# Performance work log

Hardware: AMD Instinct MI355X
Metric: run time of the kernel (lower is better)

## Reference

```python
import jax, jax.numpy as jnp
import numpy as np


def conv2d(x, w, b=None, pad=0):
    out = jax.lax.conv_general_dilated(x, w, (1, 1), [(pad, pad), (pad, pad)],
                                       dimension_numbers=('NCHW', 'OIHW', 'NCHW'))
    if b is not None:
        out = out + b[None, :, None, None]
    return out


def resb(x, w1, w2):
    y = conv2d(x, w1, pad=1)
    y = jnp.where(y > 0, y, 0.1 * y)  # LeakyReLU(0.1)
    y = conv2d(y, w2, pad=1)
    return y + x


def fepam(Q, S, R, px, py):
    # Q: (b,C,h,w); S: (b,C,H,W); R: (b,vC,H,W); px,py: (b,h,w,k) int coords into (H,W)
    b, C, h, w = Q.shape
    Ws = S.shape[3]
    vC = R.shape[1]
    k = px.shape[-1]
    idx = (px.reshape(b, -1) * Ws + py.reshape(b, -1))  # (b, h*w*k) flat spatial index
    Key = jnp.take_along_axis(S.reshape(b, C, -1), idx[:, None, :], axis=2).reshape(b, C, h * w, k)
    Val = jnp.take_along_axis(R.reshape(b, vC, -1), idx[:, None, :], axis=2).reshape(b, vC, h * w, k)
    Qv = Q.transpose(0, 2, 3, 1).reshape(b, h * w, C)
    score = jnp.einsum('bqc,bcqk->bqk', Qv, Key)          # (b, h*w, k)
    attn = jax.nn.softmax(score, axis=-1)
    buf = jnp.einsum('bqk,bvqk->bqv', attn, Val)          # (b, h*w, vC)
    return buf.reshape(b, h, w, vC).transpose(0, 3, 1, 2)


def setup_inputs() -> dict:
    key = jax.random.key(0)
    ks = jax.random.split(key, 24)
    b, C, h, w = 2, 32, 128, 128
    H, W = 512, 512
    ct, cout, kk = 16, 32, 64
    s = 0.05
    inp = {
        'lr0': jax.random.normal(ks[0], (b, C, h, w), jnp.float32),
        'lr1': jax.random.normal(ks[1], (b, C, h, w), jnp.float32),
        'lr2': jax.random.normal(ks[2], (b, C, h, w), jnp.float32),
        'hr_in': jax.random.normal(ks[3], (b, C, H, W), jnp.float32),
        'wl1': jax.random.normal(ks[4], (C, C, 3, 3), jnp.float32) * s,
        'wl2': jax.random.normal(ks[5], (C, C, 3, 3), jnp.float32) * s,
        'wh1': jax.random.normal(ks[6], (C, C, 3, 3), jnp.float32) * s,
        'wh2': jax.random.normal(ks[7], (C, C, 3, 3), jnp.float32) * s,
        'wq': jax.random.normal(ks[8], (ct, C, 1, 1), jnp.float32) * s,
        'bq': jax.random.normal(ks[9], (ct,), jnp.float32) * s,
        'wk': jax.random.normal(ks[10], (ct, C, 1, 1), jnp.float32) * s,
        'bk': jax.random.normal(ks[11], (ct,), jnp.float32) * s,
        'whk': jax.random.normal(ks[12], (ct, C, 1, 1), jnp.float32) * s,
        'bhk': jax.random.normal(ks[13], (ct,), jnp.float32) * s,
        'wf': jax.random.normal(ks[14], (cout, C * 3 + C, 1, 1), jnp.float32) * s,
        'bf': jax.random.normal(ks[15], (cout,), jnp.float32) * s,
        'px0': jax.random.randint(ks[16], (b, h, w, kk), 0, h, jnp.int64),
        'py0': jax.random.randint(ks[17], (b, h, w, kk), 0, w, jnp.int64),
        'px1': jax.random.randint(ks[18], (b, h, w, kk), 0, h, jnp.int64),
        'py1': jax.random.randint(ks[19], (b, h, w, kk), 0, w, jnp.int64),
        'px2': jax.random.randint(ks[20], (b, h, w, kk), 0, H, jnp.int64),
        'py2': jax.random.randint(ks[21], (b, h, w, kk), 0, W, jnp.int64),
        'is_training': 1,
    }
    return inp


def reference(lr0, lr1, lr2, hr_in, wl1, wl2, wh1, wh2, wq, bq, wk, bk, whk, bhk, wf, bf,
              px0, py0, px1, py1, px2, py2, is_training):
    lb0 = resb(lr0, wl1, wl2)
    lb1 = resb(lr1, wl1, wl2)
    lb2 = resb(lr2, wl1, wl2)
    hb = resb(hr_in, wh1, wh2)
    Q = conv2d(lb0, wq, bq)
    S1 = conv2d(lb1, wk, bk)
    S2 = conv2d(lb2, wk, bk)
    S3 = conv2d(hb, whk, bhk)
    b1 = fepam(Q, S1, lr1, px0, py0)
    b2 = fepam(Q, S2, lr2, px1, py1)
    b3 = fepam(Q, S3, hr_in, px2, py2)
    out = conv2d(jnp.concatenate([b1, b2, b3, lb0], axis=1), wf, bf)
    return out
```

## Files before the change

### kernel.cpp

```cpp
#include <hip/hip_runtime.h>
#include <hip/hip_bf16.h>

typedef short bfv8 __attribute__((ext_vector_type(8)));
typedef float f4v __attribute__((ext_vector_type(4)));
typedef float f2v __attribute__((ext_vector_type(2)));

static __device__ __forceinline__ unsigned short f2bf(float f) {
  unsigned u = __float_as_uint(f);
  unsigned r = (u + 0x7FFFu + ((u >> 16) & 1u)) >> 16;
  return (unsigned short)r;
}
static __device__ __forceinline__ unsigned pack2bf(float lo, float hi) {
  return (unsigned)f2bf(lo) | ((unsigned)f2bf(hi) << 16);
}
static __device__ __forceinline__ unsigned pack4fp8(float a, float b, float c, float d) {
  int w = __builtin_amdgcn_cvt_pk_fp8_f32(a, b, 0, 0);
  w = __builtin_amdgcn_cvt_pk_fp8_f32(c, d, w, 1);
  return (unsigned)w;
}


struct B3  { const unsigned short* p[3]; };
struct F3  { const float* p[3]; };
struct OB3 { unsigned short* p[3]; };
struct OF3 { float* p[3]; };
struct OC3 { unsigned char* p[3]; };

__global__ __launch_bounds__(256) void wconv_bf16_kernel(
    const float* __restrict__ wl1, const float* __restrict__ wl2,
    const float* __restrict__ wh1, const float* __restrict__ wh2,
    const float* __restrict__ whk, const float* __restrict__ wq,
    const float* __restrict__ wk,
    unsigned short* __restrict__ ol1, unsigned short* __restrict__ ol2,
    unsigned short* __restrict__ oh1, unsigned short* __restrict__ oh2,
    unsigned short* __restrict__ ok, unsigned short* __restrict__ oq,
    unsigned short* __restrict__ okk,
    const int* __restrict__ pxprobe, int* __restrict__ flag)
{
  int i = blockIdx.x * 256 + threadIdx.x;
  int y = blockIdx.y;
  if (y < 4) {
    const float* w = y == 0 ? wl1 : y == 1 ? wl2 : y == 2 ? wh1 : wh2;
    unsigned short* o = y == 0 ? ol1 : y == 1 ? ol2 : y == 2 ? oh1 : oh2;
    if (i < 9216) {
      int t = i / 1024, rem = i % 1024, co = rem >> 5, ci = rem & 31;
      o[i] = f2bf(w[(co * 32 + ci) * 9 + t]);
    }
  } else if (y == 4) {
    if (i < 512) ok[i] = f2bf(whk[i]);
    else if (i < 1024) oq[i - 512] = f2bf(wq[i - 512]);
    else if (i < 1536) okk[i - 1024] = f2bf(wk[i - 1024]);
  } else if (blockIdx.x == 0) {
    __shared__ int s;
    if (threadIdx.x == 0) s = 0;
    __syncthreads();
    if (pxprobe[2 * threadIdx.x + 1] != 0) atomicOr(&s, 1);
    __syncthreads();
    if (threadIdx.x == 0) *flag = (s == 0) ? 1 : 0;
  }
}

__global__ __launch_bounds__(256) void hrc_kernel(
    const float* __restrict__ x, unsigned short* __restrict__ o,
    unsigned char* __restrict__ kv)
{
  int p = blockIdx.x * 256 + threadIdx.x;
  int bb = p >> 18, pp = p & 262143;
  const float* xb = x + ((size_t)bb * 32) * 262144 + pp;
  float f[32];
  unsigned short v[32];
#pragma unroll
  for (int c = 0; c < 32; ++c) { f[c] = xb[(size_t)c * 262144]; v[c] = f2bf(f[c]); }
  uint4* op = (uint4*)(o + (size_t)p * 32);
#pragma unroll
  for (int q = 0; q < 4; ++q) op[q] = ((uint4*)v)[q];
  unsigned w8[8];
#pragma unroll
  for (int d = 0; d < 8; ++d)
    w8[d] = pack4fp8(f[4 * d], f[4 * d + 1], f[4 * d + 2], f[4 * d + 3]);
  uint4* o8p = (uint4*)(kv + (size_t)p * 64 + 16);
  o8p[0] = ((uint4*)w8)[0];
  o8p[1] = ((uint4*)w8)[1];
}

__global__ __launch_bounds__(256) void lrprep_kernel(F3 xs, OB3 ob, OC3 kvs)
{
  int tn = blockIdx.y;
  int p = blockIdx.x * 256 + threadIdx.x;
  int bb = p >> 14, pp = p & 16383;
  const float* xb = xs.p[tn] + ((size_t)bb * 32) * 16384 + pp;
  float f[32];
  unsigned short v[32];
#pragma unroll
  for (int c = 0; c < 32; ++c) { f[c] = xb[(size_t)c * 16384]; v[c] = f2bf(f[c]); }
  uint4* bp = (uint4*)(ob.p[tn] + (size_t)p * 32);
#pragma unroll
  for (int q = 0; q < 4; ++q) bp[q] = ((uint4*)v)[q];
  unsigned char* kv = kvs.p[tn];
  if (kv) {
    unsigned w8[8];
#pragma unroll
    for (int d = 0; d < 8; ++d)
      w8[d] = pack4fp8(f[4 * d], f[4 * d + 1], f[4 * d + 2], f[4 * d + 3]);
    uint4* o8p = (uint4*)(kv + (size_t)p * 64 + 16);
    o8p[0] = ((uint4*)w8)[0];
    o8p[1] = ((uint4*)w8)[1];
  }
}

template <int N, int MODE>
__global__ __launch_bounds__(256, 2) void conv_mfma_kernel(
    B3 xs, const unsigned short* __restrict__ WB, B3 resb,
    B3 pwb, F3 pbias, OB3 outb, OF3 outf)
{
  __shared__ uint4 smem_[2640];
  unsigned char* smem = (unsigned char*)smem_;
  const int NN = N * N;
  const int bx0 = blockIdx.x * 64, by0 = blockIdx.y * 8;
  const int tn = (N == 512) ? 0 : (blockIdx.z >> 1);
  const int bb = (N == 512) ? blockIdx.z : (blockIdx.z & 1);
  const int tid = threadIdx.x;
  const int w = tid >> 6, lane = tid & 63;
  const int l15 = lane & 15, ch = lane >> 4;

  bfv8 wa[9][2];
#pragma unroll
  for (int t = 0; t < 9; ++t)
#pragma unroll
    for (int j = 0; j < 2; ++j)
      wa[t][j] = *(const bfv8*)(WB + t * 1024 + (16 * j + l15) * 32 + ch * 8);

  const unsigned short* Xb = xs.p[tn] + (size_t)bb * NN * 32;
  for (int g = tid; g < 2640; g += 256) {
    int row = g / 264, rem = g - row * 264;
    int px = rem >> 2, c4 = rem & 3;
    int gy = by0 + row - 1, gx = bx0 + px - 1;
    uint4 v = {0u, 0u, 0u, 0u};
    if (gy >= 0 && gy < N && gx >= 0 && gx < N)
      v = *(const uint4*)(Xb + (size_t)(gy * N + gx) * 32 + c4 * 8);
    int byt = (row * 4224 + px * 64 + c4 * 16) ^ ((px & 7) << 4);
    *(uint4*)(smem + byt) = v;
  }
  __syncthreads();

  f4v acc[2][8];
#pragma unroll
  for (int j = 0; j < 2; ++j)
#pragma unroll
    for (int f = 0; f < 8; ++f) acc[j][f] = (f4v){0.f, 0.f, 0.f, 0.f};

#pragma unroll
  for (int dy = 0; dy < 3; ++dy)
#pragma unroll
    for (int dx = 0; dx < 3; ++dx)
#pragma unroll
      for (int f = 0; f < 8; ++f) {
        const int hrow = 2 * w + (f >> 2) + dy;
        const int xh = 16 * (f & 3) + l15 + dx;
        const int byt = (hrow * 4224 + xh * 64 + ch * 16) ^ ((xh & 7) << 4);
        bfv8 b = *(bfv8*)(smem + byt);
        acc[0][f] = __builtin_amdgcn_mfma_f32_16x16x32_bf16(wa[dy * 3 + dx][0], b, acc[0][f], 0, 0, 0);
        acc[1][f] = __builtin_amdgcn_mfma_f32_16x16x32_bf16(wa[dy * 3 + dx][1], b, acc[1][f], 0, 0, 0);
      }

  if (MODE == 0) {
    unsigned short* ob = outb.p[tn] + (size_t)bb * NN * 32;
#pragma unroll
    for (int j = 0; j < 2; ++j)
#pragma unroll
      for (int f = 0; f < 8; ++f) {
        const int gy = by0 + 2 * w + (f >> 2);
        const int gx = bx0 + 16 * (f & 3) + l15;
        const int co0 = 16 * j + ch * 4;
        unsigned short o[4];
#pragma unroll
        for (int i = 0; i < 4; ++i) {
          float a = acc[j][f][i];
          a = a > 0.f ? a : 0.1f * a;
          o[i] = f2bf(a);
        }
        *(uint2*)(ob + (size_t)(gy * N + gx) * 32 + co0) = *(uint2*)o;
      }
  } else {
    const unsigned short* rb = resb.p[tn] + (size_t)bb * NN * 32;
#pragma unroll
    for (int j = 0; j < 2; ++j)
#pragma unroll
      for (int f = 0; f < 8; ++f) {
        const int gy = by0 + 2 * w + (f >> 2);
        const int gx = bx0 + 16 * (f & 3) + l15;
        const int co0 = 16 * j + ch * 4;
        uint2 r = *(const uint2*)(rb + (size_t)(gy * N + gx) * 32 + co0);
        acc[j][f][0] += __uint_as_float(r.x << 16);
        acc[j][f][1] += __uint_as_float(r.x & 0xFFFF0000u);
        acc[j][f][2] += __uint_as_float(r.y << 16);
        acc[j][f][3] += __uint_as_float(r.y & 0xFFFF0000u);
      }
    if (MODE == 3 && tn == 0) {
      float* lb = outf.p[0] + (size_t)bb * NN * 32;
#pragma unroll
      for (int j = 0; j < 2; ++j)
#pragma unroll
        for (int f = 0; f < 8; ++f) {
          const int gy = by0 + 2 * w + (f >> 2);
          const int gx = bx0 + 16 * (f & 3) + l15;
          const int co0 = 16 * j + ch * 4;
          float o[4] = {acc[j][f][0], acc[j][f][1], acc[j][f][2], acc[j][f][3]};
          *(float4*)(lb + (size_t)(gy * N + gx) * 32 + co0) = *(float4*)o;
        }
    }
    __syncthreads();
#pragma unroll
    for (int j = 0; j < 2; ++j)
#pragma unroll
      for (int f = 0; f < 8; ++f) {
        const int rl = 2 * w + (f >> 2);
        const int xl = 16 * (f & 3) + l15;
        const int co0 = 16 * j + ch * 4;
        unsigned short o[4];
#pragma unroll
        for (int i = 0; i < 4; ++i) o[i] = f2bf(acc[j][f][i]);
        int byt = ((rl * 4096 + xl * 64 + ((co0 >> 3) << 4)) ^ ((xl & 7) << 4)) + (co0 & 7) * 2;
        *(uint2*)(smem + byt) = *(uint2*)o;
      }
    __syncthreads();
    bfv8 pka = *(const bfv8*)(pwb.p[tn] + l15 * 32 + ch * 8);
    float4 bv = *(const float4*)(pbias.p[tn] + ch * 4);
#pragma unroll
    for (int f = 0; f < 8; ++f) {
      const int rl = 2 * w + (f >> 2);
      const int xl = 16 * (f & 3) + l15;
      const int byt = (rl * 4096 + xl * 64 + ch * 16) ^ ((xl & 7) << 4);
      bfv8 b = *(bfv8*)(smem + byt);
      f4v a2 = __builtin_amdgcn_mfma_f32_16x16x32_bf16(pka, b, (f4v){0.f, 0.f, 0.f, 0.f}, 0, 0, 0);
      const int gy = by0 + rl, gx = bx0 + xl;
      if (MODE == 3 && tn == 0) {
        float* Pq = outf.p[1] + (size_t)bb * ((size_t)NN * 16);
        float o[4] = {a2[0] + bv.x, a2[1] + bv.y, a2[2] + bv.z, a2[3] + bv.w};
        *(float4*)(Pq + (size_t)(gy * N + gx) * 16 + ch * 4) = *(float4*)o;
      } else {
        unsigned char* KV = (unsigned char*)outb.p[tn];
        unsigned wd = pack4fp8(a2[0] + bv.x, a2[1] + bv.y, a2[2] + bv.z, a2[3] + bv.w);
        *(unsigned*)(KV + ((size_t)bb * NN + (size_t)(gy * N + gx)) * 64 + ch * 4) = wd;
      }
    }
  }
}

__global__ __launch_bounds__(256) void fepam_kernel(
    const float* __restrict__ Qt, const unsigned char* __restrict__ KV,
    const int* __restrict__ px, const int* __restrict__ py,
    const int* __restrict__ idxflag, float* __restrict__ out, int Ws, int HWs)
{
  __shared__ unsigned pv[4][64][17];
  const int wv = threadIdx.x >> 6;
  const int lane = threadIdx.x & 63;
  const int wid = (blockIdx.x * 256 + threadIdx.x) >> 6;
  const int bb = wid >> 14;
  const int f = *idxflag;
  const int j = (wid * 64 + lane) << f;
  const int sidx = px[j] * Ws + py[j];

  const unsigned char* rec = KV + ((size_t)bb * HWs + sidx) * 64;
  uint4 kw  = *(const uint4*)rec;
  uint4 vw0 = *(const uint4*)(rec + 16);
  uint4 vw1 = *(const uint4*)(rec + 32);

  const float* qp = Qt + (size_t)wid * 16;
  float qreg[16];
#pragma unroll
  for (int q = 0; q < 4; ++q) ((float4*)qreg)[q] = ((const float4*)qp)[q];

  unsigned karr[4] = {kw.x, kw.y, kw.z, kw.w};
  float score = 0.f;
#pragma unroll
  for (int d = 0; d < 4; ++d) {
    f2v lo = __builtin_amdgcn_cvt_pk_f32_fp8((int)karr[d], 0);
    f2v hi = __builtin_amdgcn_cvt_pk_f32_fp8((int)karr[d], 1);
    score = fmaf(qreg[4 * d],     lo[0], score);
    score = fmaf(qreg[4 * d + 1], lo[1], score);
    score = fmaf(qreg[4 * d + 2], hi[0], score);
    score = fmaf(qreg[4 * d + 3], hi[1], score);
  }
  float e = __expf(fminf(score, 80.f));
  float s = e;
#pragma unroll
  for (int off = 32; off; off >>= 1) s += __shfl_xor(s, off);

  unsigned varr[8] = {vw0.x, vw0.y, vw0.z, vw0.w, vw1.x, vw1.y, vw1.z, vw1.w};
#pragma unroll
  for (int d = 0; d < 8; ++d) {
    f2v lo = __builtin_amdgcn_cvt_pk_f32_fp8((int)varr[d], 0);
    f2v hi = __builtin_amdgcn_cvt_pk_f32_fp8((int)varr[d], 1);
    unsigned ulo0 = __float_as_uint(e * lo[0]) + 0x8000u;
    unsigned ulo1 = __float_as_uint(e * lo[1]) + 0x8000u;
    unsigned uhi0 = __float_as_uint(e * hi[0]) + 0x8000u;
    unsigned uhi1 = __float_as_uint(e * hi[1]) + 0x8000u;
    pv[wv][lane][2 * d]     = (ulo0 >> 16) | (ulo1 & 0xFFFF0000u);
    pv[wv][lane][2 * d + 1] = (uhi0 >> 16) | (uhi1 & 0xFFFF0000u);
  }
  __syncthreads();

  const int c = lane & 31, h = lane >> 5;
  const int wsel = c >> 1;
  const unsigned sh = (c & 1) ? 0u : 16u;
  float val = 0.f;
#pragma unroll
  for (int i = 0; i < 32; ++i) {
    unsigned u = pv[wv][h * 32 + i][wsel];
    val += __uint_as_float((u << sh) & 0xFFFF0000u);
  }
  val += __shfl_xor(val, 32);
  if (lane < 32) out[(size_t)wid * 32 + c] = val / s;
}

__global__ __launch_bounds__(256) void final_conv_kernel(
    const float* __restrict__ bt1, const float* __restrict__ bt2,
    const float* __restrict__ bt3, const float* __restrict__ lb0,
    const float* __restrict__ wf, const float* __restrict__ bfb,
    float* __restrict__ out)
{
  __shared__ uint4 smem_[1544];
  unsigned char* smem = (unsigned char*)smem_;
  const int tid = threadIdx.x;
  const int px0 = blockIdx.x * 64;

  {
    const int pxl = tid >> 2, c0 = (tid & 3) * 8;
    const float* srcs[4] = {bt1, bt2, bt3, lb0};
#pragma unroll
    for (int q = 0; q < 4; ++q) {
      const float* sp = srcs[q] + (size_t)(px0 + pxl) * 32 + c0;
      float4 a = ((const float4*)sp)[0];
      float4 b = ((const float4*)sp)[1];
      unsigned pk[4] = {pack2bf(a.x, a.y), pack2bf(a.z, a.w),
                        pack2bf(b.x, b.y), pack2bf(b.z, b.w)};
      int byt = (pxl * 256 + q * 64 + c0 * 2) ^ ((pxl & 7) << 4);
      *(uint4*)(smem + byt) = *(uint4*)pk;
    }
    const int co = tid >> 3, cw = (tid & 7) * 16;
    const float* wp = wf + co * 128 + cw;
    float4 w0 = ((const float4*)wp)[0], w1 = ((const float4*)wp)[1];
    float4 w2 = ((const float4*)wp)[2], w3 = ((const float4*)wp)[3];
    unsigned pk0[4] = {pack2bf(w0.x, w0.y), pack2bf(w0.z, w0.w),
                       pack2bf(w1.x, w1.y), pack2bf(w1.z, w1.w)};
    unsigned pk1[4] = {pack2bf(w2.x, w2.y), pack2bf(w2.z, w2.w),
                       pack2bf(w3.x, w3.y), pack2bf(w3.z, w3.w)};
    int b0 = 16384 + ((co * 256 + cw * 2) ^ ((co & 7) << 4));
    int b1 = 16384 + ((co * 256 + cw * 2 + 16) ^ ((co & 7) << 4));
    *(uint4*)(smem + b0) = *(uint4*)pk0;
    *(uint4*)(smem + b1) = *(uint4*)pk1;
    if (tid < 32) *(float*)(smem + 24576 + tid * 4) = bfb[tid];
  }
  __syncthreads();

  const int w = tid >> 6, lane = tid & 63;
  const int l15 = lane & 15, ch = lane >> 4;
  const int pxl = w * 16 + l15;

  f4v acc[2] = {(f4v){0.f, 0.f, 0.f, 0.f}, (f4v){0.f, 0.f, 0.f, 0.f}};
#pragma unroll
  for (int kb = 0; kb < 4; ++kb) {
    bfv8 b = *(bfv8*)(smem + ((pxl * 256 + kb * 64 + ch * 16) ^ ((pxl & 7) << 4)));
#pragma unroll
    for (int j = 0; j < 2; ++j) {
      const int co = 16 * j + l15;
      bfv8 a = *(bfv8*)(smem + 16384 + ((co * 256 + kb * 64 + ch * 16) ^ ((co & 7) << 4)));
      acc[j] = __builtin_amdgcn_mfma_f32_16x16x32_bf16(a, b, acc[j], 0, 0, 0);
    }
  }

  const int p = px0 + pxl;
  const int bb = p >> 14, pp = p & 16383;
#pragma unroll
  for (int j = 0; j < 2; ++j)
#pragma unroll
    for (int i = 0; i < 4; ++i) {
      const int co = 16 * j + ch * 4 + i;
      float bias = *(float*)(smem + 24576 + co * 4);
      out[((size_t)(bb * 32 + co)) * 16384 + pp] = acc[j][i] + bias;
    }
}

extern "C" void kernel_launch(void* const* d_in, const int* in_sizes, int n_in,
                              void* d_out, int out_size, void* d_ws, size_t ws_size,
                              hipStream_t stream)
{
  const float* lr0 = (const float*)d_in[0];
  const float* lr1 = (const float*)d_in[1];
  const float* lr2 = (const float*)d_in[2];
  const float* hr  = (const float*)d_in[3];
  const float* wl1 = (const float*)d_in[4];
  const float* wl2 = (const float*)d_in[5];
  const float* wh1 = (const float*)d_in[6];
  const float* wh2 = (const float*)d_in[7];
  const float* wq  = (const float*)d_in[8];
  const float* bq  = (const float*)d_in[9];
  const float* wk  = (const float*)d_in[10];
  const float* bk  = (const float*)d_in[11];
  const float* whk = (const float*)d_in[12];
  const float* bhk = (const float*)d_in[13];
  const float* wf  = (const float*)d_in[14];
  const float* bf  = (const float*)d_in[15];
  const int* px0 = (const int*)d_in[16];
  const int* py0 = (const int*)d_in[17];
  const int* px1 = (const int*)d_in[18];
  const int* py1 = (const int*)d_in[19];
  const int* px2 = (const int*)d_in[20];
  const int* py2 = (const int*)d_in[21];
  float* out = (float*)d_out;
  float* ws = (float*)d_ws;

  unsigned char*  KV3 = (unsigned char*)ws;
  unsigned short* YC  = (unsigned short*)(ws + 8388608);
  unsigned short* HRC = (unsigned short*)(ws + 16777216);
  unsigned short* LRC = (unsigned short*)(ws + 25165824);
  unsigned short* YLC = (unsigned short*)(ws + 26738688);
  unsigned char*  KV1 = (unsigned char*)(ws + 28311552);
  unsigned char*  KV2 = (unsigned char*)(ws + 28835840);
  float* QT  = ws + 29360128;
  float* LB0 = ws + 30408704;
  float* BT1 = ws + 33030144;
  float* BT2 = ws + 34078720;
  float* BT3 = ws + 35127296;
  unsigned short* WBL1 = (unsigned short*)(ws + 36175872);
  unsigned short* WBL2 = (unsigned short*)(ws + 36180480);
  unsigned short* WBH1 = (unsigned short*)(ws + 36185088);
  unsigned short* WBH2 = (unsigned short*)(ws + 36189696);
  unsigned short* WHKB = (unsigned short*)(ws + 36194304);
  unsigned short* WQB  = (unsigned short*)(ws + 36194560);
  unsigned short* WKB  = (unsigned short*)(ws + 36194816);
  int* IDXFLAG = (int*)(ws + 36195072);

  unsigned short* LRC0 = LRC;
  unsigned short* LRC1 = LRC + 1048576;
  unsigned short* LRC2 = LRC + 2097152;
  unsigned short* YLC0 = YLC;
  unsigned short* YLC1 = YLC + 1048576;
  unsigned short* YLC2 = YLC + 2097152;

  B3 bnone{};
  F3 fnone{};
  OB3 obnone{};
  OF3 ofnone{};

  static hipStream_t s2 = nullptr;
  static hipEvent_t eA = nullptr, eB = nullptr, eS = nullptr;
  if (s2 == nullptr) {
    hipStreamCreateWithFlags(&s2, hipStreamNonBlocking);
    hipEventCreateWithFlags(&eA, hipEventDisableTiming);
    hipEventCreateWithFlags(&eB, hipEventDisableTiming);
    hipEventCreateWithFlags(&eS, hipEventDisableTiming);
  }

  wconv_bf16_kernel<<<dim3(36, 6), 256, 0, stream>>>(
      wl1, wl2, wh1, wh2, whk, wq, wk,
      WBL1, WBL2, WBH1, WBH2, WHKB, WQB, WKB, px0, IDXFLAG);
  hipEventRecord(eA, stream);

  hipStreamWaitEvent(s2, eA, 0);
  hrc_kernel<<<2048, 256, 0, s2>>>(hr, HRC, KV3);
  conv_mfma_kernel<512, 0><<<dim3(8, 64, 2), 256, 0, s2>>>(
      B3{{HRC}}, WBH1, bnone, bnone, fnone, OB3{{YC}}, ofnone);
  conv_mfma_kernel<512, 2><<<dim3(8, 64, 2), 256, 0, s2>>>(
      B3{{YC}}, WBH2, B3{{HRC}}, B3{{WHKB}}, F3{{bhk}},
      OB3{{(unsigned short*)KV3}}, ofnone);

  lrprep_kernel<<<dim3(128, 3), 256, 0, stream>>>(
      F3{{lr0, lr1, lr2}}, OB3{{LRC0, LRC1, LRC2}}, OC3{{nullptr, KV1, KV2}});
  conv_mfma_kernel<128, 0><<<dim3(2, 16, 6), 256, 0, stream>>>(
      B3{{LRC0, LRC1, LRC2}}, WBL1, bnone, bnone, fnone,
      OB3{{YLC0, YLC1, YLC2}}, ofnone);
  conv_mfma_kernel<128, 3><<<dim3(2, 16, 6), 256, 0, stream>>>(
      B3{{YLC0, YLC1, YLC2}}, WBL2, B3{{LRC0, LRC1, LRC2}},
      B3{{WQB, WKB, WKB}}, F3{{bq, bk, bk}},
      OB3{{nullptr, (unsigned short*)KV1, (unsigned short*)KV2}},
      OF3{{LB0, QT, nullptr}});
  hipEventRecord(eB, stream);

  hipStreamWaitEvent(s2, eB, 0);
  fepam_kernel<<<8192, 256, 0, s2>>>(QT, KV3, px2, py2, IDXFLAG, BT3, 512, 262144);
  hipEventRecord(eS, s2);

  fepam_kernel<<<8192, 256, 0, stream>>>(QT, KV1, px0, py0, IDXFLAG, BT1, 128, 16384);
  fepam_kernel<<<8192, 256, 0, stream>>>(QT, KV2, px1, py1, IDXFLAG, BT2, 128, 16384);

  hipStreamWaitEvent(stream, eS, 0);
  final_conv_kernel<<<512, 256, 0, stream>>>(BT1, BT2, BT3, LB0, wf, bf, out);
}
```

Measured before the change: 192.1 us.

## Split HR conv and fepam3 per batch to pipeline across streams

Splits the second high-res conv into two per-batch launches, each signalling its own event. The third fepam is split per batch on the main stream, so batch 0 attention can start as soon as its KV3 half is ready, while batch 1's conv still runs on the side stream. The lr-side fepams now run first on the main stream. This lets the high-res conv tail overlap with attention work, at the cost of extra launches and smaller grids.

```diff
diff --git a/kernel.cpp b/kernel.cpp
--- a/kernel.cpp
+++ b/kernel.cpp
@@ -250,12 +250,13 @@
 __global__ __launch_bounds__(256) void fepam_kernel(
     const float* __restrict__ Qt, const unsigned char* __restrict__ KV,
     const int* __restrict__ px, const int* __restrict__ py,
-    const int* __restrict__ idxflag, float* __restrict__ out, int Ws, int HWs)
+    const int* __restrict__ idxflag, float* __restrict__ out,
+    int Ws, int HWs, int wid0)
 {
   __shared__ unsigned pv[4][64][17];
   const int wv = threadIdx.x >> 6;
   const int lane = threadIdx.x & 63;
-  const int wid = (blockIdx.x * 256 + threadIdx.x) >> 6;
+  const int wid = wid0 + ((blockIdx.x * 256 + threadIdx.x) >> 6);
   const int bb = wid >> 14;
   const int f = *idxflag;
   const int j = (wid * 64 + lane) << f;
@@ -439,18 +440,20 @@
   unsigned short* YLC1 = YLC + 1048576;
   unsigned short* YLC2 = YLC + 2097152;
 
+  const size_t NN512 = 512 * 512;
+
   B3 bnone{};
   F3 fnone{};
   OB3 obnone{};
   OF3 ofnone{};
 
   static hipStream_t s2 = nullptr;
-  static hipEvent_t eA = nullptr, eB = nullptr, eS = nullptr;
+  static hipEvent_t eA = nullptr, e20 = nullptr, e21 = nullptr;
   if (s2 == nullptr) {
     hipStreamCreateWithFlags(&s2, hipStreamNonBlocking);
     hipEventCreateWithFlags(&eA, hipEventDisableTiming);
-    hipEventCreateWithFlags(&eB, hipEventDisableTiming);
-    hipEventCreateWithFlags(&eS, hipEventDisableTiming);
+    hipEventCreateWithFlags(&e20, hipEventDisableTiming);
+    hipEventCreateWithFlags(&e21, hipEventDisableTiming);
   }
 
   wconv_bf16_kernel<<<dim3(36, 6), 256, 0, stream>>>(
@@ -462,9 +465,14 @@
   hrc_kernel<<<2048, 256, 0, s2>>>(hr, HRC, KV3);
   conv_mfma_kernel<512, 0><<<dim3(8, 64, 2), 256, 0, s2>>>(
       B3{{HRC}}, WBH1, bnone, bnone, fnone, OB3{{YC}}, ofnone);
-  conv_mfma_kernel<512, 2><<<dim3(8, 64, 2), 256, 0, s2>>>(
+  conv_mfma_kernel<512, 2><<<dim3(8, 64, 1), 256, 0, s2>>>(
       B3{{YC}}, WBH2, B3{{HRC}}, B3{{WHKB}}, F3{{bhk}},
       OB3{{(unsigned short*)KV3}}, ofnone);
+  hipEventRecord(e20, s2);
+  conv_mfma_kernel<512, 2><<<dim3(8, 64, 1), 256, 0, s2>>>(
+      B3{{YC + NN512 * 32}}, WBH2, B3{{HRC + NN512 * 32}}, B3{{WHKB}}, F3{{bhk}},
+      OB3{{(unsigned short*)(KV3 + NN512 * 64)}}, ofnone);
+  hipEventRecord(e21, s2);
 
   lrprep_kernel<<<dim3(128, 3), 256, 0, stream>>>(
       F3{{lr0, lr1, lr2}}, OB3{{LRC0, LRC1, LRC2}}, OC3{{nullptr, KV1, KV2}});
@@ -476,15 +484,13 @@
       B3{{WQB, WKB, WKB}}, F3{{bq, bk, bk}},
       OB3{{nullptr, (unsigned short*)KV1, (unsigned short*)KV2}},
       OF3{{LB0, QT, nullptr}});
-  hipEventRecord(eB, stream);
-
-  hipStreamWaitEvent(s2, eB, 0);
-  fepam_kernel<<<8192, 256, 0, s2>>>(QT, KV3, px2, py2, IDXFLAG, BT3, 512, 262144);
-  hipEventRecord(eS, s2);
-
-  fepam_kernel<<<8192, 256, 0, stream>>>(QT, KV1, px0, py0, IDXFLAG, BT1, 128, 16384);
-  fepam_kernel<<<8192, 256, 0, stream>>>(QT, KV2, px1, py1, IDXFLAG, BT2, 128, 16384);
-
-  hipStreamWaitEvent(stream, eS, 0);
+
+  fepam_kernel<<<8192, 256, 0, stream>>>(QT, KV1, px0, py0, IDXFLAG, BT1, 128, 16384, 0);
+  fepam_kernel<<<8192, 256, 0, stream>>>(QT, KV2, px1, py1, IDXFLAG, BT2, 128, 16384, 0);
+  hipStreamWaitEvent(stream, e20, 0);
+  fepam_kernel<<<4096, 256, 0, stream>>>(QT, KV3, px2, py2, IDXFLAG, BT3, 512, 262144, 0);
+  hipStreamWaitEvent(stream, e21, 0);
+  fepam_kernel<<<4096, 256, 0, stream>>>(QT, KV3, px2, py2, IDXFLAG, BT3, 512, 262144, 16384);
+
   final_conv_kernel<<<512, 256, 0, stream>>>(BT1, BT2, BT3, LB0, wf, bf, out);
 }
```

Result: slower. 202.1 us (+5.2%).
